# Kernel tuning notes

Measured on AMD Instinct MI355X. Metric: run time of the kernel, lower is better.

Reference implementation:

```python
import jax, jax.numpy as jnp
import numpy as np

HEADS = 8
EPS = 1e-4

def pixel_norm(x):
    # faithful to source: mean over dim=1 (token axis for [B,T,C] tensors)
    return x / jnp.sqrt(jnp.mean(x * x, axis=1, keepdims=True) + EPS)

def setup_inputs() -> dict:
    key = jax.random.key(0)
    ks = jax.random.split(key, 6)
    B, T, C = 4, 2048, 512
    s = 1.0 / np.sqrt(C)
    return {
        "hidden_states": jax.random.normal(ks[0], (B, T, C), jnp.float32),
        "Wq": jax.random.normal(ks[1], (C, C), jnp.float32) * s,
        "Wk": jax.random.normal(ks[2], (C, C), jnp.float32) * s,
        "Wv": jax.random.normal(ks[3], (C, C), jnp.float32) * s,
        "Wo": jax.random.normal(ks[4], (C, C), jnp.float32) * s,
        "bo": jnp.zeros((C,), jnp.float32),
    }

def reference(hidden_states, Wq, Wk, Wv, Wo, bo):
    B, T, C = hidden_states.shape
    H = HEADS
    d = C // H
    scale = 1.0 / np.sqrt(d)  # attn.scale = head_dim**-0.5
    residual = hidden_states

    q = pixel_norm(hidden_states @ Wq)  # [B,T,C]
    k = pixel_norm(hidden_states @ Wk)
    v = pixel_norm(hidden_states @ Wv)

    # head_to_batch_dim: [B,T,C] -> [B,H,T,d]
    def split_heads(x):
        return x.reshape(B, T, H, d).transpose(0, 2, 1, 3)
    q, k, v = split_heads(q), split_heads(k), split_heads(v)

    scores = jnp.einsum("bhqd,bhkd->bhqk", q, k) * scale
    probs = jax.nn.softmax(scores, axis=-1)
    out = jnp.einsum("bhqk,bhkd->bhqd", probs, v)  # [B,H,T,d]

    # batch_to_head_dim: [B,H,T,d] -> [B,T,C]
    out = out.transpose(0, 2, 1, 3).reshape(B, T, C)
    out = out @ Wo + bo  # to_out[0]; to_out[1] is dropout (identity in eval)
    out = out + residual  # residual_connection
    return out  # rescale_output_factor = 1.0
```

## Files before the change

### kernel.cpp

```cpp
#include <hip/hip_runtime.h>

#define Tt 2048
#define Cc 512
#define Bb 4
#define BC (Bb * Cc)

typedef __attribute__((ext_vector_type(4))) float f32x4;
typedef __attribute__((ext_vector_type(8))) _Float16 f16x8;
typedef __attribute__((ext_vector_type(4))) _Float16 f16x4;

__global__ __launch_bounds__(256) void wsetup(
    const float* __restrict__ Wq, const float* __restrict__ Wk,
    const float* __restrict__ Wv, const float* __restrict__ Wo,
    _Float16* __restrict__ Wt)
{
    const int z = blockIdx.y;
    const float* W = (z == 0) ? Wq : (z == 1) ? Wk : (z == 2) ? Wv : Wo;
    const int k0 = (blockIdx.x >> 3) * 64, n0 = (blockIdx.x & 7) * 64;
    const int tid = threadIdx.x;
    __shared__ float tile[64][65];

#pragma unroll
    for (int i = 0; i < 4; ++i) {
        const int idx = i * 256 + tid;
        const int kr = idx >> 4, c4 = idx & 15;
        float4 v = *(const float4*)&W[(size_t)(k0 + kr) * Cc + n0 + c4 * 4];
        tile[kr][c4 * 4 + 0] = v.x; tile[kr][c4 * 4 + 1] = v.y;
        tile[kr][c4 * 4 + 2] = v.z; tile[kr][c4 * 4 + 3] = v.w;
    }
    __syncthreads();
#pragma unroll
    for (int i = 0; i < 4; ++i) {
        const int idx = i * 256 + tid;
        const int nr = idx >> 4, k4 = idx & 15;
        f16x4 o;
        o[0] = (_Float16)tile[k4 * 4 + 0][nr];
        o[1] = (_Float16)tile[k4 * 4 + 1][nr];
        o[2] = (_Float16)tile[k4 * 4 + 2][nr];
        o[3] = (_Float16)tile[k4 * 4 + 3][nr];
        *(f16x4*)&Wt[((size_t)(z * 512 + n0 + nr)) * Cc + k0 + k4 * 4] = o;
    }
}

__global__ __launch_bounds__(256, 3) void qkv_mfma(
    const float* __restrict__ HS, const _Float16* __restrict__ Wt,
    _Float16* __restrict__ Qf, _Float16* __restrict__ Kf,
    _Float16* __restrict__ Vf, float* __restrict__ colsum)
{
    const int mt = blockIdx.x;
    const int nt = blockIdx.y;
    const int z  = blockIdx.z;
    _Float16* Out = (z == 0) ? Qf : (z == 1) ? Kf : Vf;

    const int tid = threadIdx.x;
    const int wave = tid >> 6, lane = tid & 63;
    const int quad = lane >> 4, lm = lane & 15;
    const int wm = (wave & 1) * 64, wn = (wave >> 1) * 64;

    __shared__ _Float16 sA[128 * 40];
    __shared__ _Float16 sB[128 * 40];

    f32x4 acc[4][4];
#pragma unroll
    for (int mf = 0; mf < 4; ++mf)
#pragma unroll
        for (int nf = 0; nf < 4; ++nf) acc[mf][nf] = (f32x4){0.f, 0.f, 0.f, 0.f};

    const int r2 = tid >> 1, kc = (tid & 1) * 16;
    const float* ga = HS + (size_t)(mt * 128 + r2) * Cc + kc;
    const _Float16* gb = Wt + ((size_t)(z * 512 + nt * 128 + r2)) * Cc + kc;

    for (int k0 = 0; k0 < Cc; k0 += 32) {
        __syncthreads();
        {
            float4 a0 = *(const float4*)&ga[k0];
            float4 a1 = *(const float4*)&ga[k0 + 4];
            float4 a2 = *(const float4*)&ga[k0 + 8];
            float4 a3 = *(const float4*)&ga[k0 + 12];
            f16x8 h0, h1;
            h0[0] = (_Float16)a0.x; h0[1] = (_Float16)a0.y;
            h0[2] = (_Float16)a0.z; h0[3] = (_Float16)a0.w;
            h0[4] = (_Float16)a1.x; h0[5] = (_Float16)a1.y;
            h0[6] = (_Float16)a1.z; h0[7] = (_Float16)a1.w;
            h1[0] = (_Float16)a2.x; h1[1] = (_Float16)a2.y;
            h1[2] = (_Float16)a2.z; h1[3] = (_Float16)a2.w;
            h1[4] = (_Float16)a3.x; h1[5] = (_Float16)a3.y;
            h1[6] = (_Float16)a3.z; h1[7] = (_Float16)a3.w;
            *(f16x8*)&sA[r2 * 40 + kc]     = h0;
            *(f16x8*)&sA[r2 * 40 + kc + 8] = h1;
            *(f16x8*)&sB[r2 * 40 + kc]     = *(const f16x8*)&gb[k0];
            *(f16x8*)&sB[r2 * 40 + kc + 8] = *(const f16x8*)&gb[k0 + 8];
        }
        __syncthreads();

        f16x8 ah[4], bh[4];
#pragma unroll
        for (int mf = 0; mf < 4; ++mf)
            ah[mf] = *(const f16x8*)&sA[(wm + mf * 16 + lm) * 40 + quad * 8];
#pragma unroll
        for (int nf = 0; nf < 4; ++nf)
            bh[nf] = *(const f16x8*)&sB[(wn + nf * 16 + lm) * 40 + quad * 8];
#pragma unroll
        for (int mf = 0; mf < 4; ++mf)
#pragma unroll
            for (int nf = 0; nf < 4; ++nf)
                acc[mf][nf] = __builtin_amdgcn_mfma_f32_16x16x32_f16(ah[mf], bh[nf], acc[mf][nf], 0, 0, 0);
    }

    const int bidx = mt >> 4;
#pragma unroll
    for (int nf = 0; nf < 4; ++nf) {
        float cs = 0.f;
#pragma unroll
        for (int mf = 0; mf < 4; ++mf)
#pragma unroll
            for (int r = 0; r < 4; ++r) {
                const float v = acc[mf][nf][r];
                const size_t idx =
                    (size_t)(mt * 128 + wm + mf * 16 + quad * 4 + r) * Cc +
                    nt * 128 + wn + nf * 16 + lm;
                Out[idx] = (_Float16)v;
                cs += v * v;
            }
        cs += __shfl_xor(cs, 16, 64);
        cs += __shfl_xor(cs, 32, 64);
        if (lane < 16)
            atomicAdd(&colsum[(size_t)z * BC + bidx * Cc + nt * 128 + wn + nf * 16 + lane], cs);
    }
}

__global__ void inv_norm_kernel(const float* __restrict__ colsum,
                                float* __restrict__ inv)
{
    const int i = blockIdx.x * blockDim.x + threadIdx.x;
    if (i < 3 * BC) inv[i] = rsqrtf(colsum[i] * (1.0f / Tt) + 1e-4f);
}

__global__ __launch_bounds__(256) void norm_vt(
    const _Float16* __restrict__ V, _Float16* __restrict__ VT)
{
    const int blk = blockIdx.x;
    const int b = blk >> 8, ct = (blk >> 5) & 7, tt = blk & 31;
    const int t0 = tt * 64, c0 = ct * 64;
    const int tid = threadIdx.x;

    __shared__ _Float16 tile[64 * 72];

#pragma unroll
    for (int i = 0; i < 2; ++i) {
        const int idx = i * 256 + tid;
        const int tr = idx >> 3, c8 = (idx & 7) * 8;
        *(f16x8*)&tile[tr * 72 + c8] =
            *(const f16x8*)&V[(size_t)(b * Tt + t0 + tr) * Cc + c0 + c8];
    }
    __syncthreads();
#pragma unroll
    for (int i = 0; i < 2; ++i) {
        const int idx = i * 256 + tid;
        const int cr = idx >> 3, t8 = (idx & 7) * 8;
        f16x8 o;
#pragma unroll
        for (int j = 0; j < 8; ++j) o[j] = tile[(t8 + j) * 72 + cr];
        *(f16x8*)&VT[(size_t)(b * Cc + c0 + cr) * Tt + t0 + t8] = o;
    }
}

#define LSTR 72

__global__ __launch_bounds__(256, 2) void attn_mfma(
    const _Float16* __restrict__ Qf, const _Float16* __restrict__ Kf,
    const _Float16* __restrict__ VT, const float* __restrict__ inv,
    _Float16* __restrict__ AO)
{
    const int qt = blockIdx.x;
    const int bh = blockIdx.y;
    const int b = bh >> 3, h = bh & 7;
    const int tid = threadIdx.x;
    const int wave = tid >> 6, lane = tid & 63;
    const int quad = lane >> 4, lm = lane & 15;

    __shared__ _Float16 sK[64 * LSTR];
    __shared__ _Float16 sVT[64 * LSTR];
    __shared__ _Float16 sP[4 * 32 * LSTR];
    _Float16* myP = sP + wave * 32 * LSTR;

    f16x8 qb[2][2];
    {
        const float* iqp = inv + b * Cc + h * 64;
        const float* ikp = inv + BC + b * Cc + h * 64;
#pragma unroll
        for (int qf = 0; qf < 2; ++qf) {
            const int row = qt * 128 + wave * 32 + qf * 16 + lm;
#pragma unroll
            for (int ks = 0; ks < 2; ++ks) {
                const int d0 = ks * 32 + quad * 8;
                f16x8 qv = *(const f16x8*)&Qf[(size_t)(b * Tt + row) * Cc + h * 64 + d0];
#pragma unroll
                for (int j = 0; j < 8; ++j) {
                    const float f = (float)qv[j] * iqp[d0 + j] * ikp[d0 + j] * 0.125f;
                    qb[qf][ks][j] = (_Float16)f;
                }
            }
        }
    }

    f32x4 o[4][2];
#pragma unroll
    for (int cf = 0; cf < 4; ++cf)
#pragma unroll
        for (int qf = 0; qf < 2; ++qf) o[cf][qf] = (f32x4){0.f, 0.f, 0.f, 0.f};
    float ls[2] = {0.f, 0.f};

    const int sr0 = tid >> 3, sc0 = (tid & 7) * 8;
    const int sr1 = sr0 + 32;
    const _Float16* gK = Kf + (size_t)b * Tt * Cc + h * 64;
    const _Float16* gV = VT + ((size_t)b * Cc + h * 64) * Tt;

    f16x8 rk0, rk1, rv0, rv1;
    {
        rk0 = *(const f16x8*)&gK[(size_t)sr0 * Cc + sc0];
        rk1 = *(const f16x8*)&gK[(size_t)sr1 * Cc + sc0];
        rv0 = *(const f16x8*)&gV[(size_t)sr0 * Tt + sc0];
        rv1 = *(const f16x8*)&gV[(size_t)sr1 * Tt + sc0];
    }

    for (int kt = 0; kt < 32; ++kt) {
        __syncthreads();
        *(f16x8*)&sK[sr0 * LSTR + sc0] = rk0;
        *(f16x8*)&sK[sr1 * LSTR + sc0] = rk1;
        *(f16x8*)&sVT[sr0 * LSTR + sc0] = rv0;
        *(f16x8*)&sVT[sr1 * LSTR + sc0] = rv1;
        __syncthreads();

        if (kt < 31) {
            const int t0 = (kt + 1) * 64;
            rk0 = *(const f16x8*)&gK[(size_t)(t0 + sr0) * Cc + sc0];
            rk1 = *(const f16x8*)&gK[(size_t)(t0 + sr1) * Cc + sc0];
            rv0 = *(const f16x8*)&gV[(size_t)sr0 * Tt + t0 + sc0];
            rv1 = *(const f16x8*)&gV[(size_t)sr1 * Tt + t0 + sc0];
        }

        f32x4 st[4][2];
#pragma unroll
        for (int kf = 0; kf < 4; ++kf)
#pragma unroll
            for (int qf = 0; qf < 2; ++qf) st[kf][qf] = (f32x4){0.f, 0.f, 0.f, 0.f};
#pragma unroll
        for (int ks = 0; ks < 2; ++ks) {
            f16x8 ka[4];
#pragma unroll
            for (int kf = 0; kf < 4; ++kf)
                ka[kf] = *(const f16x8*)&sK[(kf * 16 + lm) * LSTR + ks * 32 + quad * 8];
#pragma unroll
            for (int kf = 0; kf < 4; ++kf)
#pragma unroll
                for (int qf = 0; qf < 2; ++qf)
                    st[kf][qf] = __builtin_amdgcn_mfma_f32_16x16x32_f16(ka[kf], qb[qf][ks], st[kf][qf], 0, 0, 0);
        }

#pragma unroll
        for (int kf = 0; kf < 4; ++kf)
#pragma unroll
            for (int qf = 0; qf < 2; ++qf) {
                f16x4 pk;
#pragma unroll
                for (int r = 0; r < 4; ++r) {
                    const float p = __expf(st[kf][qf][r]);
                    ls[qf] += p;
                    pk[r] = (_Float16)p;
                }
                *(f16x4*)&myP[(qf * 16 + lm) * LSTR + kf * 16 + quad * 4] = pk;
            }

#pragma unroll
        for (int ks = 0; ks < 2; ++ks) {
            f16x8 pb[2];
#pragma unroll
            for (int qf = 0; qf < 2; ++qf)
                pb[qf] = *(const f16x8*)&myP[(qf * 16 + lm) * LSTR + ks * 32 + quad * 8];
            f16x8 va[4];
#pragma unroll
            for (int cf = 0; cf < 4; ++cf)
                va[cf] = *(const f16x8*)&sVT[(cf * 16 + lm) * LSTR + ks * 32 + quad * 8];
#pragma unroll
            for (int cf = 0; cf < 4; ++cf)
#pragma unroll
                for (int qf = 0; qf < 2; ++qf)
                    o[cf][qf] = __builtin_amdgcn_mfma_f32_16x16x32_f16(va[cf], pb[qf], o[cf][qf], 0, 0, 0);
        }
    }

    float il[2];
#pragma unroll
    for (int qf = 0; qf < 2; ++qf) {
        float s = ls[qf];
        s += __shfl_xor(s, 16, 64);
        s += __shfl_xor(s, 32, 64);
        il[qf] = 1.0f / s;
    }
    const float* ivp = inv + 2 * BC + b * Cc + h * 64;
    float iv[4][4];
#pragma unroll
    for (int cf = 0; cf < 4; ++cf) {
        float4 t = *(const float4*)&ivp[cf * 16 + quad * 4];
        iv[cf][0] = t.x; iv[cf][1] = t.y; iv[cf][2] = t.z; iv[cf][3] = t.w;
    }
#pragma unroll
    for (int qf = 0; qf < 2; ++qf) {
        const size_t row = (size_t)(b * Tt + qt * 128 + wave * 32 + qf * 16 + lm);
#pragma unroll
        for (int cf = 0; cf < 4; ++cf) {
            f16x4 pk;
#pragma unroll
            for (int r = 0; r < 4; ++r)
                pk[r] = (_Float16)(o[cf][qf][r] * il[qf] * iv[cf][r]);
            *(f16x4*)&AO[row * Cc + h * 64 + cf * 16 + quad * 4] = pk;
        }
    }
}

__global__ __launch_bounds__(256, 2) void out_mfma(
    const _Float16* __restrict__ AO, const _Float16* __restrict__ Wt,
    const float* __restrict__ bo, const float* __restrict__ HS,
    float* __restrict__ Outp)
{
    const int mt = blockIdx.x;
    const int nt = blockIdx.y;
    const int tid = threadIdx.x;
    const int wave = tid >> 6, lane = tid & 63;
    const int quad = lane >> 4, lm = lane & 15;
    const int wm = (wave & 1) * 32, wn = (wave >> 1) * 64;

    __shared__ _Float16 sA[64 * 40];
    __shared__ _Float16 sB[128 * 40];

    f32x4 acc[2][4];
#pragma unroll
    for (int mf = 0; mf < 2; ++mf)
#pragma unroll
        for (int nf = 0; nf < 4; ++nf) acc[mf][nf] = (f32x4){0.f, 0.f, 0.f, 0.f};

    const int ra = tid >> 2, ka = (tid & 3) * 8;
    const int rb = tid >> 1, kb = (tid & 1) * 16;
    const _Float16* gah = AO + (size_t)(mt * 64 + ra) * Cc + ka;
    const _Float16* gbh = Wt + ((size_t)(3 * 512 + nt * 128 + rb)) * Cc + kb;

    for (int k0 = 0; k0 < Cc; k0 += 32) {
        __syncthreads();
        {
            *(f16x8*)&sA[ra * 40 + ka] = *(const f16x8*)&gah[k0];
            *(f16x8*)&sB[rb * 40 + kb]     = *(const f16x8*)&gbh[k0];
            *(f16x8*)&sB[rb * 40 + kb + 8] = *(const f16x8*)&gbh[k0 + 8];
        }
        __syncthreads();

        f16x8 ah[2], bh[4];
#pragma unroll
        for (int mf = 0; mf < 2; ++mf)
            ah[mf] = *(const f16x8*)&sA[(wm + mf * 16 + lm) * 40 + quad * 8];
#pragma unroll
        for (int nf = 0; nf < 4; ++nf)
            bh[nf] = *(const f16x8*)&sB[(wn + nf * 16 + lm) * 40 + quad * 8];
#pragma unroll
        for (int mf = 0; mf < 2; ++mf)
#pragma unroll
            for (int nf = 0; nf < 4; ++nf)
                acc[mf][nf] = __builtin_amdgcn_mfma_f32_16x16x32_f16(ah[mf], bh[nf], acc[mf][nf], 0, 0, 0);
    }

#pragma unroll
    for (int mf = 0; mf < 2; ++mf)
#pragma unroll
        for (int r = 0; r < 4; ++r) {
            const size_t m = (size_t)(mt * 64 + wm + mf * 16 + quad * 4 + r);
#pragma unroll
            for (int nf = 0; nf < 4; ++nf) {
                const int col = nt * 128 + wn + nf * 16 + lm;
                Outp[m * Cc + col] = acc[mf][nf][r] + bo[col] + HS[m * Cc + col];
            }
        }
}

extern "C" void kernel_launch(void* const* d_in, const int* in_sizes, int n_in,
                              void* d_out, int out_size, void* d_ws,
                              size_t ws_size, hipStream_t stream)
{
    const float* HS = (const float*)d_in[0];
    const float* Wq = (const float*)d_in[1];
    const float* Wk = (const float*)d_in[2];
    const float* Wv = (const float*)d_in[3];
    const float* Wo = (const float*)d_in[4];
    const float* bo = (const float*)d_in[5];
    float* out = (float*)d_out;

    const size_t SZ = (size_t)Bb * Tt * Cc;
    _Float16* Qf  = (_Float16*)d_ws;
    _Float16* Kf  = Qf + SZ;
    _Float16* Vf  = Kf + SZ;
    _Float16* VTh = Vf + SZ;
    _Float16* AO  = VTh + SZ;
    _Float16* Wt  = AO + SZ;
    float* colsum = (float*)(Wt + 4 * Cc * Cc);
    float* inv    = colsum + 3 * BC;

    hipMemsetAsync(colsum, 0, 3 * BC * sizeof(float), stream);

    wsetup<<<dim3(64, 4), 256, 0, stream>>>(Wq, Wk, Wv, Wo, Wt);

    qkv_mfma<<<dim3(64, 4, 3), 256, 0, stream>>>(HS, Wt, Qf, Kf, Vf, colsum);

    inv_norm_kernel<<<(3 * BC + 255) / 256, 256, 0, stream>>>(colsum, inv);

    norm_vt<<<1024, 256, 0, stream>>>(Vf, VTh);

    attn_mfma<<<dim3(16, 32), 256, 0, stream>>>(Qf, Kf, VTh, inv, AO);

    out_mfma<<<dim3(128, 4), 256, 0, stream>>>(AO, Wt, bo, HS, out);
}
```

Baseline: 184.0 us.

## Use 8 waves of 16 query rows per attention block with exp2 softmax

The attention kernel now runs 512 threads per block, and each wave owns 16 query rows instead of 32. Per-thread accumulator and score registers are halved, and the block is declared for higher occupancy. The softmax switches to exp2, with log2(e) folded into the Q prescale, and uses packed round-toward-zero f16 conversion. In exchange, each K/V tile loaded into LDS is shared across more waves, but every wave reloads the V fragments for only half the MFMA work, and barriers now synchronize 8 waves.

```diff
diff --git a/kernel.cpp b/kernel.cpp
--- a/kernel.cpp
+++ b/kernel.cpp
@@ -8,6 +8,7 @@
 typedef __attribute__((ext_vector_type(4))) float f32x4;
 typedef __attribute__((ext_vector_type(8))) _Float16 f16x8;
 typedef __attribute__((ext_vector_type(4))) _Float16 f16x4;
+typedef __attribute__((ext_vector_type(2))) _Float16 f16x2;
 
 __global__ __launch_bounds__(256) void wsetup(
     const float* __restrict__ Wq, const float* __restrict__ Wk,
@@ -167,7 +168,7 @@
 
 #define LSTR 72
 
-__global__ __launch_bounds__(256, 2) void attn_mfma(
+__global__ __launch_bounds__(512, 4) void attn_mfma(
     const _Float16* __restrict__ Qf, const _Float16* __restrict__ Kf,
     const _Float16* __restrict__ VT, const float* __restrict__ inv,
     _Float16* __restrict__ AO)
@@ -181,70 +182,56 @@
 
     __shared__ _Float16 sK[64 * LSTR];
     __shared__ _Float16 sVT[64 * LSTR];
-    __shared__ _Float16 sP[4 * 32 * LSTR];
-    _Float16* myP = sP + wave * 32 * LSTR;
-
-    f16x8 qb[2][2];
+    __shared__ _Float16 sP[8 * 16 * LSTR];
+    _Float16* myP = sP + wave * 16 * LSTR;
+
+    f16x8 qb[2];
     {
         const float* iqp = inv + b * Cc + h * 64;
         const float* ikp = inv + BC + b * Cc + h * 64;
-#pragma unroll
-        for (int qf = 0; qf < 2; ++qf) {
-            const int row = qt * 128 + wave * 32 + qf * 16 + lm;
-#pragma unroll
-            for (int ks = 0; ks < 2; ++ks) {
-                const int d0 = ks * 32 + quad * 8;
-                f16x8 qv = *(const f16x8*)&Qf[(size_t)(b * Tt + row) * Cc + h * 64 + d0];
-#pragma unroll
-                for (int j = 0; j < 8; ++j) {
-                    const float f = (float)qv[j] * iqp[d0 + j] * ikp[d0 + j] * 0.125f;
-                    qb[qf][ks][j] = (_Float16)f;
-                }
+        const int row = qt * 128 + wave * 16 + lm;
+#pragma unroll
+        for (int ks = 0; ks < 2; ++ks) {
+            const int d0 = ks * 32 + quad * 8;
+            f16x8 qv = *(const f16x8*)&Qf[(size_t)(b * Tt + row) * Cc + h * 64 + d0];
+#pragma unroll
+            for (int j = 0; j < 8; ++j) {
+                const float f = (float)qv[j] * iqp[d0 + j] * ikp[d0 + j] * 0.18033688011f;
+                qb[ks][j] = (_Float16)f;
             }
         }
     }
 
-    f32x4 o[4][2];
-#pragma unroll
-    for (int cf = 0; cf < 4; ++cf)
-#pragma unroll
-        for (int qf = 0; qf < 2; ++qf) o[cf][qf] = (f32x4){0.f, 0.f, 0.f, 0.f};
-    float ls[2] = {0.f, 0.f};
-
-    const int sr0 = tid >> 3, sc0 = (tid & 7) * 8;
-    const int sr1 = sr0 + 32;
+    f32x4 o[4];
+#pragma unroll
+    for (int cf = 0; cf < 4; ++cf) o[cf] = (f32x4){0.f, 0.f, 0.f, 0.f};
+    float ls = 0.f;
+
+    const int sr = tid >> 3, sc = (tid & 7) * 8;
     const _Float16* gK = Kf + (size_t)b * Tt * Cc + h * 64;
     const _Float16* gV = VT + ((size_t)b * Cc + h * 64) * Tt;
 
-    f16x8 rk0, rk1, rv0, rv1;
+    f16x8 rk, rv;
     {
-        rk0 = *(const f16x8*)&gK[(size_t)sr0 * Cc + sc0];
-        rk1 = *(const f16x8*)&gK[(size_t)sr1 * Cc + sc0];
-        rv0 = *(const f16x8*)&gV[(size_t)sr0 * Tt + sc0];
-        rv1 = *(const f16x8*)&gV[(size_t)sr1 * Tt + sc0];
+        rk = *(const f16x8*)&gK[(size_t)sr * Cc + sc];
+        rv = *(const f16x8*)&gV[(size_t)sr * Tt + sc];
     }
 
     for (int kt = 0; kt < 32; ++kt) {
         __syncthreads();
-        *(f16x8*)&sK[sr0 * LSTR + sc0] = rk0;
-        *(f16x8*)&sK[sr1 * LSTR + sc0] = rk1;
-        *(f16x8*)&sVT[sr0 * LSTR + sc0] = rv0;
-        *(f16x8*)&sVT[sr1 * LSTR + sc0] = rv1;
+        *(f16x8*)&sK[sr * LSTR + sc] = rk;
+        *(f16x8*)&sVT[sr * LSTR + sc] = rv;
         __syncthreads();
 
         if (kt < 31) {
             const int t0 = (kt + 1) * 64;
-            rk0 = *(const f16x8*)&gK[(size_t)(t0 + sr0) * Cc + sc0];
-            rk1 = *(const f16x8*)&gK[(size_t)(t0 + sr1) * Cc + sc0];
-            rv0 = *(const f16x8*)&gV[(size_t)sr0 * Tt + t0 + sc0];
-            rv1 = *(const f16x8*)&gV[(size_t)sr1 * Tt + t0 + sc0];
-        }
-
-        f32x4 st[4][2];
-#pragma unroll
-        for (int kf = 0; kf < 4; ++kf)
-#pragma unroll
-            for (int qf = 0; qf < 2; ++qf) st[kf][qf] = (f32x4){0.f, 0.f, 0.f, 0.f};
+            rk = *(const f16x8*)&gK[(size_t)(t0 + sr) * Cc + sc];
+            rv = *(const f16x8*)&gV[(size_t)sr * Tt + t0 + sc];
+        }
+
+        f32x4 st[4];
+#pragma unroll
+        for (int kf = 0; kf < 4; ++kf) st[kf] = (f32x4){0.f, 0.f, 0.f, 0.f};
 #pragma unroll
         for (int ks = 0; ks < 2; ++ks) {
             f16x8 ka[4];
@@ -253,50 +240,42 @@
                 ka[kf] = *(const f16x8*)&sK[(kf * 16 + lm) * LSTR + ks * 32 + quad * 8];
 #pragma unroll
             for (int kf = 0; kf < 4; ++kf)
-#pragma unroll
-                for (int qf = 0; qf < 2; ++qf)
-                    st[kf][qf] = __builtin_amdgcn_mfma_f32_16x16x32_f16(ka[kf], qb[qf][ks], st[kf][qf], 0, 0, 0);
-        }
-
-#pragma unroll
-        for (int kf = 0; kf < 4; ++kf)
-#pragma unroll
-            for (int qf = 0; qf < 2; ++qf) {
-                f16x4 pk;
-#pragma unroll
-                for (int r = 0; r < 4; ++r) {
-                    const float p = __expf(st[kf][qf][r]);
-                    ls[qf] += p;
-                    pk[r] = (_Float16)p;
-                }
-                *(f16x4*)&myP[(qf * 16 + lm) * LSTR + kf * 16 + quad * 4] = pk;
-            }
+                st[kf] = __builtin_amdgcn_mfma_f32_16x16x32_f16(ka[kf], qb[ks], st[kf], 0, 0, 0);
+        }
+
+#pragma unroll
+        for (int kf = 0; kf < 4; ++kf) {
+            const float p0 = __builtin_amdgcn_exp2f(st[kf][0]);
+            const float p1 = __builtin_amdgcn_exp2f(st[kf][1]);
+            const float p2 = __builtin_amdgcn_exp2f(st[kf][2]);
+            const float p3 = __builtin_amdgcn_exp2f(st[kf][3]);
+            ls += (p0 + p1) + (p2 + p3);
+            const f16x2 lo = __builtin_bit_cast(f16x2, __builtin_amdgcn_cvt_pkrtz(p0, p1));
+            const f16x2 hi = __builtin_bit_cast(f16x2, __builtin_amdgcn_cvt_pkrtz(p2, p3));
+            f16x4 pk;
+            pk[0] = lo[0]; pk[1] = lo[1]; pk[2] = hi[0]; pk[3] = hi[1];
+            *(f16x4*)&myP[lm * LSTR + kf * 16 + quad * 4] = pk;
+        }
 
 #pragma unroll
         for (int ks = 0; ks < 2; ++ks) {
-            f16x8 pb[2];
-#pragma unroll
-            for (int qf = 0; qf < 2; ++qf)
-                pb[qf] = *(const f16x8*)&myP[(qf * 16 + lm) * LSTR + ks * 32 + quad * 8];
+            f16x8 pb = *(const f16x8*)&myP[lm * LSTR + ks * 32 + quad * 8];
             f16x8 va[4];
 #pragma unroll
             for (int cf = 0; cf < 4; ++cf)
                 va[cf] = *(const f16x8*)&sVT[(cf * 16 + lm) * LSTR + ks * 32 + quad * 8];
 #pragma unroll
             for (int cf = 0; cf < 4; ++cf)
-#pragma unroll
-                for (int qf = 0; qf < 2; ++qf)
-                    o[cf][qf] = __builtin_amdgcn_mfma_f32_16x16x32_f16(va[cf], pb[qf], o[cf][qf], 0, 0, 0);
-        }
-    }
-
-    float il[2];
-#pragma unroll
-    for (int qf = 0; qf < 2; ++qf) {
-        float s = ls[qf];
+                o[cf] = __builtin_amdgcn_mfma_f32_16x16x32_f16(va[cf], pb, o[cf], 0, 0, 0);
+        }
+    }
+
+    float il;
+    {
+        float s = ls;
         s += __shfl_xor(s, 16, 64);
         s += __shfl_xor(s, 32, 64);
-        il[qf] = 1.0f / s;
+        il = 1.0f / s;
     }
     const float* ivp = inv + 2 * BC + b * Cc + h * 64;
     float iv[4][4];
@@ -305,15 +284,14 @@
         float4 t = *(const float4*)&ivp[cf * 16 + quad * 4];
         iv[cf][0] = t.x; iv[cf][1] = t.y; iv[cf][2] = t.z; iv[cf][3] = t.w;
     }
-#pragma unroll
-    for (int qf = 0; qf < 2; ++qf) {
-        const size_t row = (size_t)(b * Tt + qt * 128 + wave * 32 + qf * 16 + lm);
+    {
+        const size_t row = (size_t)(b * Tt + qt * 128 + wave * 16 + lm);
 #pragma unroll
         for (int cf = 0; cf < 4; ++cf) {
             f16x4 pk;
 #pragma unroll
             for (int r = 0; r < 4; ++r)
-                pk[r] = (_Float16)(o[cf][qf][r] * il[qf] * iv[cf][r]);
+                pk[r] = (_Float16)(o[cf][r] * il * iv[cf][r]);
             *(f16x4*)&AO[row * Cc + h * 64 + cf * 16 + quad * 4] = pk;
         }
     }
@@ -403,7 +381,7 @@
     float* colsum = (float*)(Wt + 4 * Cc * Cc);
     float* inv    = colsum + 3 * BC;
 
-    hipMemsetAsync(colsum, 0, 3 * BC * sizeof(float), stream);
+    (void)hipMemsetAsync(colsum, 0, 3 * BC * sizeof(float), stream);
 
     wsetup<<<dim3(64, 4), 256, 0, stream>>>(Wq, Wk, Wv, Wo, Wt);
 
@@ -413,7 +391,7 @@
 
     norm_vt<<<1024, 256, 0, stream>>>(Vf, VTh);
 
-    attn_mfma<<<dim3(16, 32), 256, 0, stream>>>(Qf, Kf, VTh, inv, AO);
+    attn_mfma<<<dim3(16, 32), 512, 0, stream>>>(Qf, Kf, VTh, inv, AO);
 
     out_mfma<<<dim3(128, 4), 256, 0, stream>>>(AO, Wt, bo, HS, out);
 }
```

Result: slower. 189.1 us (+2.8%).

## Split attention key loop across two wave groups with LDS reduction, use exp2

Applied to the files above, without the earlier changes.

The attention block grows from 256 to 512 threads. Two groups of four waves each process alternating 64-key tiles for the same 128 queries, each with its own K/V shared buffers. The partial outputs and row sums are merged through shared memory at the end. Separately, the softmax scale is folded with log2(e) so exp2 can replace expf, and packed RTZ conversions build the fp16 probabilities. This doubles the waves working on the serial key loop, at the cost of more LDS, a final reduction step and possible occupancy limits.

```diff
diff --git a/kernel.cpp b/kernel.cpp
--- a/kernel.cpp
+++ b/kernel.cpp
@@ -8,6 +8,7 @@
 typedef __attribute__((ext_vector_type(4))) float f32x4;
 typedef __attribute__((ext_vector_type(8))) _Float16 f16x8;
 typedef __attribute__((ext_vector_type(4))) _Float16 f16x4;
+typedef __attribute__((ext_vector_type(2))) _Float16 f16x2;
 
 __global__ __launch_bounds__(256) void wsetup(
     const float* __restrict__ Wq, const float* __restrict__ Wk,
@@ -167,7 +168,7 @@
 
 #define LSTR 72
 
-__global__ __launch_bounds__(256, 2) void attn_mfma(
+__global__ __launch_bounds__(512, 4) void attn_mfma(
     const _Float16* __restrict__ Qf, const _Float16* __restrict__ Kf,
     const _Float16* __restrict__ VT, const float* __restrict__ inv,
     _Float16* __restrict__ AO)
@@ -177,12 +178,15 @@
     const int b = bh >> 3, h = bh & 7;
     const int tid = threadIdx.x;
     const int wave = tid >> 6, lane = tid & 63;
+    const int wg = wave & 3, grp = wave >> 2;
     const int quad = lane >> 4, lm = lane & 15;
 
-    __shared__ _Float16 sK[64 * LSTR];
-    __shared__ _Float16 sVT[64 * LSTR];
-    __shared__ _Float16 sP[4 * 32 * LSTR];
+    __shared__ _Float16 sK[2][64 * LSTR];
+    __shared__ _Float16 sVT[2][64 * LSTR];
+    __shared__ _Float16 sP[8 * 32 * LSTR];
     _Float16* myP = sP + wave * 32 * LSTR;
+    _Float16* sKg = sK[grp];
+    _Float16* sVg = sVT[grp];
 
     f16x8 qb[2][2];
     {
@@ -190,14 +194,14 @@
         const float* ikp = inv + BC + b * Cc + h * 64;
 #pragma unroll
         for (int qf = 0; qf < 2; ++qf) {
-            const int row = qt * 128 + wave * 32 + qf * 16 + lm;
+            const int row = qt * 128 + wg * 32 + qf * 16 + lm;
 #pragma unroll
             for (int ks = 0; ks < 2; ++ks) {
                 const int d0 = ks * 32 + quad * 8;
                 f16x8 qv = *(const f16x8*)&Qf[(size_t)(b * Tt + row) * Cc + h * 64 + d0];
 #pragma unroll
                 for (int j = 0; j < 8; ++j) {
-                    const float f = (float)qv[j] * iqp[d0 + j] * ikp[d0 + j] * 0.125f;
+                    const float f = (float)qv[j] * iqp[d0 + j] * ikp[d0 + j] * 0.18033688011f;
                     qb[qf][ks][j] = (_Float16)f;
                 }
             }
@@ -211,33 +215,35 @@
         for (int qf = 0; qf < 2; ++qf) o[cf][qf] = (f32x4){0.f, 0.f, 0.f, 0.f};
     float ls[2] = {0.f, 0.f};
 
-    const int sr0 = tid >> 3, sc0 = (tid & 7) * 8;
+    const int g256 = tid & 255;
+    const int sr0 = g256 >> 3, sc0 = (g256 & 7) * 8;
     const int sr1 = sr0 + 32;
     const _Float16* gK = Kf + (size_t)b * Tt * Cc + h * 64;
     const _Float16* gV = VT + ((size_t)b * Cc + h * 64) * Tt;
 
     f16x8 rk0, rk1, rv0, rv1;
     {
-        rk0 = *(const f16x8*)&gK[(size_t)sr0 * Cc + sc0];
-        rk1 = *(const f16x8*)&gK[(size_t)sr1 * Cc + sc0];
-        rv0 = *(const f16x8*)&gV[(size_t)sr0 * Tt + sc0];
-        rv1 = *(const f16x8*)&gV[(size_t)sr1 * Tt + sc0];
-    }
-
-    for (int kt = 0; kt < 32; ++kt) {
-        __syncthreads();
-        *(f16x8*)&sK[sr0 * LSTR + sc0] = rk0;
-        *(f16x8*)&sK[sr1 * LSTR + sc0] = rk1;
-        *(f16x8*)&sVT[sr0 * LSTR + sc0] = rv0;
-        *(f16x8*)&sVT[sr1 * LSTR + sc0] = rv1;
-        __syncthreads();
-
-        if (kt < 31) {
-            const int t0 = (kt + 1) * 64;
-            rk0 = *(const f16x8*)&gK[(size_t)(t0 + sr0) * Cc + sc0];
-            rk1 = *(const f16x8*)&gK[(size_t)(t0 + sr1) * Cc + sc0];
-            rv0 = *(const f16x8*)&gV[(size_t)sr0 * Tt + t0 + sc0];
-            rv1 = *(const f16x8*)&gV[(size_t)sr1 * Tt + t0 + sc0];
+        const int t0 = grp * 64;
+        rk0 = *(const f16x8*)&gK[(size_t)(t0 + sr0) * Cc + sc0];
+        rk1 = *(const f16x8*)&gK[(size_t)(t0 + sr1) * Cc + sc0];
+        rv0 = *(const f16x8*)&gV[(size_t)sr0 * Tt + t0 + sc0];
+        rv1 = *(const f16x8*)&gV[(size_t)sr1 * Tt + t0 + sc0];
+    }
+
+    for (int it = 0; it < 16; ++it) {
+        __syncthreads();
+        *(f16x8*)&sKg[sr0 * LSTR + sc0] = rk0;
+        *(f16x8*)&sKg[sr1 * LSTR + sc0] = rk1;
+        *(f16x8*)&sVg[sr0 * LSTR + sc0] = rv0;
+        *(f16x8*)&sVg[sr1 * LSTR + sc0] = rv1;
+        __syncthreads();
+
+        if (it < 15) {
+            const int tn = ((it + 1) * 2 + grp) * 64;
+            rk0 = *(const f16x8*)&gK[(size_t)(tn + sr0) * Cc + sc0];
+            rk1 = *(const f16x8*)&gK[(size_t)(tn + sr1) * Cc + sc0];
+            rv0 = *(const f16x8*)&gV[(size_t)sr0 * Tt + tn + sc0];
+            rv1 = *(const f16x8*)&gV[(size_t)sr1 * Tt + tn + sc0];
         }
 
         f32x4 st[4][2];
@@ -250,7 +256,7 @@
             f16x8 ka[4];
 #pragma unroll
             for (int kf = 0; kf < 4; ++kf)
-                ka[kf] = *(const f16x8*)&sK[(kf * 16 + lm) * LSTR + ks * 32 + quad * 8];
+                ka[kf] = *(const f16x8*)&sKg[(kf * 16 + lm) * LSTR + ks * 32 + quad * 8];
 #pragma unroll
             for (int kf = 0; kf < 4; ++kf)
 #pragma unroll
@@ -262,13 +268,15 @@
         for (int kf = 0; kf < 4; ++kf)
 #pragma unroll
             for (int qf = 0; qf < 2; ++qf) {
+                const float p0 = __builtin_amdgcn_exp2f(st[kf][qf][0]);
+                const float p1 = __builtin_amdgcn_exp2f(st[kf][qf][1]);
+                const float p2 = __builtin_amdgcn_exp2f(st[kf][qf][2]);
+                const float p3 = __builtin_amdgcn_exp2f(st[kf][qf][3]);
+                ls[qf] += (p0 + p1) + (p2 + p3);
+                const f16x2 lo = __builtin_bit_cast(f16x2, __builtin_amdgcn_cvt_pkrtz(p0, p1));
+                const f16x2 hi = __builtin_bit_cast(f16x2, __builtin_amdgcn_cvt_pkrtz(p2, p3));
                 f16x4 pk;
-#pragma unroll
-                for (int r = 0; r < 4; ++r) {
-                    const float p = __expf(st[kf][qf][r]);
-                    ls[qf] += p;
-                    pk[r] = (_Float16)p;
-                }
+                pk[0] = lo[0]; pk[1] = lo[1]; pk[2] = hi[0]; pk[3] = hi[1];
                 *(f16x4*)&myP[(qf * 16 + lm) * LSTR + kf * 16 + quad * 4] = pk;
             }
 
@@ -281,7 +289,7 @@
             f16x8 va[4];
 #pragma unroll
             for (int cf = 0; cf < 4; ++cf)
-                va[cf] = *(const f16x8*)&sVT[(cf * 16 + lm) * LSTR + ks * 32 + quad * 8];
+                va[cf] = *(const f16x8*)&sVg[(cf * 16 + lm) * LSTR + ks * 32 + quad * 8];
 #pragma unroll
             for (int cf = 0; cf < 4; ++cf)
 #pragma unroll
@@ -290,31 +298,56 @@
         }
     }
 
-    float il[2];
-#pragma unroll
-    for (int qf = 0; qf < 2; ++qf) {
-        float s = ls[qf];
-        s += __shfl_xor(s, 16, 64);
-        s += __shfl_xor(s, 32, 64);
-        il[qf] = 1.0f / s;
-    }
-    const float* ivp = inv + 2 * BC + b * Cc + h * 64;
-    float iv[4][4];
-#pragma unroll
-    for (int cf = 0; cf < 4; ++cf) {
-        float4 t = *(const float4*)&ivp[cf * 16 + quad * 4];
-        iv[cf][0] = t.x; iv[cf][1] = t.y; iv[cf][2] = t.z; iv[cf][3] = t.w;
-    }
-#pragma unroll
-    for (int qf = 0; qf < 2; ++qf) {
-        const size_t row = (size_t)(b * Tt + qt * 128 + wave * 32 + qf * 16 + lm);
+    float* fO = (float*)sP;
+    float* fL = (float*)sK;
+    __syncthreads();
+    if (grp == 1) {
+#pragma unroll
+        for (int cf = 0; cf < 4; ++cf)
+#pragma unroll
+            for (int qf = 0; qf < 2; ++qf)
+                *(f32x4*)&fO[wg * 2048 + (cf * 2 + qf) * 256 + lane * 4] = o[cf][qf];
+        fL[wg * 128 + lane] = ls[0];
+        fL[wg * 128 + 64 + lane] = ls[1];
+    }
+    __syncthreads();
+    if (grp == 0) {
+#pragma unroll
+        for (int cf = 0; cf < 4; ++cf)
+#pragma unroll
+            for (int qf = 0; qf < 2; ++qf) {
+                const f32x4 t = *(const f32x4*)&fO[wg * 2048 + (cf * 2 + qf) * 256 + lane * 4];
+                o[cf][qf] += t;
+            }
+        ls[0] += fL[wg * 128 + lane];
+        ls[1] += fL[wg * 128 + 64 + lane];
+
+        float il[2];
+#pragma unroll
+        for (int qf = 0; qf < 2; ++qf) {
+            float s = ls[qf];
+            s += __shfl_xor(s, 16, 64);
+            s += __shfl_xor(s, 32, 64);
+            il[qf] = 1.0f / s;
+        }
+        const float* ivp = inv + 2 * BC + b * Cc + h * 64;
+        float iv[4][4];
 #pragma unroll
         for (int cf = 0; cf < 4; ++cf) {
-            f16x4 pk;
-#pragma unroll
-            for (int r = 0; r < 4; ++r)
-                pk[r] = (_Float16)(o[cf][qf][r] * il[qf] * iv[cf][r]);
-            *(f16x4*)&AO[row * Cc + h * 64 + cf * 16 + quad * 4] = pk;
+            float4 t = *(const float4*)&ivp[cf * 16 + quad * 4];
+            iv[cf][0] = t.x; iv[cf][1] = t.y; iv[cf][2] = t.z; iv[cf][3] = t.w;
+        }
+#pragma unroll
+        for (int qf = 0; qf < 2; ++qf) {
+            const size_t row = (size_t)(b * Tt + qt * 128 + wg * 32 + qf * 16 + lm);
+#pragma unroll
+            for (int cf = 0; cf < 4; ++cf) {
+                f16x4 pk;
+#pragma unroll
+                for (int r = 0; r < 4; ++r)
+                    pk[r] = (_Float16)(o[cf][qf][r] * il[qf] * iv[cf][r]);
+                *(f16x4*)&AO[row * Cc + h * 64 + cf * 16 + quad * 4] = pk;
+            }
         }
     }
 }
@@ -403,7 +436,7 @@
     float* colsum = (float*)(Wt + 4 * Cc * Cc);
     float* inv    = colsum + 3 * BC;
 
-    hipMemsetAsync(colsum, 0, 3 * BC * sizeof(float), stream);
+    (void)hipMemsetAsync(colsum, 0, 3 * BC * sizeof(float), stream);
 
     wsetup<<<dim3(64, 4), 256, 0, stream>>>(Wq, Wk, Wv, Wo, Wt);
 
@@ -413,7 +446,7 @@
 
     norm_vt<<<1024, 256, 0, stream>>>(Vf, VTh);
 
-    attn_mfma<<<dim3(16, 32), 256, 0, stream>>>(Qf, Kf, VTh, inv, AO);
+    attn_mfma<<<dim3(16, 32), 512, 0, stream>>>(Qf, Kf, VTh, inv, AO);
 
     out_mfma<<<dim3(128, 4), 256, 0, stream>>>(AO, Wt, bo, HS, out);
 }
```

New measurement: 192.8 us. +4.8%, slower.

## Software-pipeline attention PV with double-buffered LDS, exp2 softmax, MFMA row sums

Applied to the files above, without the earlier changes.

Double-buffers the K, V^T and P tiles in shared memory so the P·V MFMAs for the previous key tile run after the QK^T MFMAs of the current tile. This lets the exponentials and matrix work of neighbouring tiles interleave. Folds log2(e) into the Q scale so it can use the hardware exp2, and packs probabilities to fp16 with cvt_pkrtz. Replaces the per-lane sum plus shuffle reduction with an MFMA against a ones vector. It also flattens the grid so consecutive blocks share the same query tile across heads. LDS use per block roughly doubles, which may limit occupancy, and round-to-zero fp16 conversion slightly changes numerics.

```diff
diff --git a/kernel.cpp b/kernel.cpp
--- a/kernel.cpp
+++ b/kernel.cpp
@@ -8,6 +8,7 @@
 typedef __attribute__((ext_vector_type(4))) float f32x4;
 typedef __attribute__((ext_vector_type(8))) _Float16 f16x8;
 typedef __attribute__((ext_vector_type(4))) _Float16 f16x4;
+typedef __attribute__((ext_vector_type(2))) _Float16 f16x2;
 
 __global__ __launch_bounds__(256) void wsetup(
     const float* __restrict__ Wq, const float* __restrict__ Wk,
@@ -172,17 +173,17 @@
     const _Float16* __restrict__ VT, const float* __restrict__ inv,
     _Float16* __restrict__ AO)
 {
-    const int qt = blockIdx.x;
-    const int bh = blockIdx.y;
+    const int bid = blockIdx.x;
+    const int qt = bid >> 5;
+    const int bh = bid & 31;
     const int b = bh >> 3, h = bh & 7;
     const int tid = threadIdx.x;
     const int wave = tid >> 6, lane = tid & 63;
     const int quad = lane >> 4, lm = lane & 15;
 
-    __shared__ _Float16 sK[64 * LSTR];
-    __shared__ _Float16 sVT[64 * LSTR];
-    __shared__ _Float16 sP[4 * 32 * LSTR];
-    _Float16* myP = sP + wave * 32 * LSTR;
+    __shared__ _Float16 sK[2][64 * LSTR];
+    __shared__ _Float16 sVT[2][64 * LSTR];
+    __shared__ _Float16 sP[2][4][32 * LSTR];
 
     f16x8 qb[2][2];
     {
@@ -197,7 +198,7 @@
                 f16x8 qv = *(const f16x8*)&Qf[(size_t)(b * Tt + row) * Cc + h * 64 + d0];
 #pragma unroll
                 for (int j = 0; j < 8; ++j) {
-                    const float f = (float)qv[j] * iqp[d0 + j] * ikp[d0 + j] * 0.125f;
+                    const float f = (float)qv[j] * iqp[d0 + j] * ikp[d0 + j] * 0.18033688011f;
                     qb[qf][ks][j] = (_Float16)f;
                 }
             }
@@ -209,7 +210,12 @@
     for (int cf = 0; cf < 4; ++cf)
 #pragma unroll
         for (int qf = 0; qf < 2; ++qf) o[cf][qf] = (f32x4){0.f, 0.f, 0.f, 0.f};
-    float ls[2] = {0.f, 0.f};
+    f32x4 ol[2];
+#pragma unroll
+    for (int qf = 0; qf < 2; ++qf) ol[qf] = (f32x4){0.f, 0.f, 0.f, 0.f};
+    f16x8 ones;
+#pragma unroll
+    for (int j = 0; j < 8; ++j) ones[j] = (_Float16)1.0f;
 
     const int sr0 = tid >> 3, sc0 = (tid & 7) * 8;
     const int sr1 = sr0 + 32;
@@ -225,11 +231,17 @@
     }
 
     for (int kt = 0; kt < 32; ++kt) {
-        __syncthreads();
-        *(f16x8*)&sK[sr0 * LSTR + sc0] = rk0;
-        *(f16x8*)&sK[sr1 * LSTR + sc0] = rk1;
-        *(f16x8*)&sVT[sr0 * LSTR + sc0] = rv0;
-        *(f16x8*)&sVT[sr1 * LSTR + sc0] = rv1;
+        const int cur = kt & 1, prv = cur ^ 1;
+        _Float16* sKc = sK[cur];
+        _Float16* sVc = sVT[cur];
+        _Float16* myPc = &sP[cur][wave][0];
+        _Float16* myPp = &sP[prv][wave][0];
+
+        __syncthreads();
+        *(f16x8*)&sKc[sr0 * LSTR + sc0] = rk0;
+        *(f16x8*)&sKc[sr1 * LSTR + sc0] = rk1;
+        *(f16x8*)&sVc[sr0 * LSTR + sc0] = rv0;
+        *(f16x8*)&sVc[sr1 * LSTR + sc0] = rv1;
         __syncthreads();
 
         if (kt < 31) {
@@ -250,7 +262,7 @@
             f16x8 ka[4];
 #pragma unroll
             for (int kf = 0; kf < 4; ++kf)
-                ka[kf] = *(const f16x8*)&sK[(kf * 16 + lm) * LSTR + ks * 32 + quad * 8];
+                ka[kf] = *(const f16x8*)&sKc[(kf * 16 + lm) * LSTR + ks * 32 + quad * 8];
 #pragma unroll
             for (int kf = 0; kf < 4; ++kf)
 #pragma unroll
@@ -258,46 +270,72 @@
                     st[kf][qf] = __builtin_amdgcn_mfma_f32_16x16x32_f16(ka[kf], qb[qf][ks], st[kf][qf], 0, 0, 0);
         }
 
+        if (kt > 0) {
+            _Float16* sVp = sVT[prv];
+#pragma unroll
+            for (int ks = 0; ks < 2; ++ks) {
+                f16x8 pb[2];
+#pragma unroll
+                for (int qf = 0; qf < 2; ++qf)
+                    pb[qf] = *(const f16x8*)&myPp[(qf * 16 + lm) * LSTR + ks * 32 + quad * 8];
+                f16x8 va[4];
+#pragma unroll
+                for (int cf = 0; cf < 4; ++cf)
+                    va[cf] = *(const f16x8*)&sVp[(cf * 16 + lm) * LSTR + ks * 32 + quad * 8];
+#pragma unroll
+                for (int cf = 0; cf < 4; ++cf)
+#pragma unroll
+                    for (int qf = 0; qf < 2; ++qf)
+                        o[cf][qf] = __builtin_amdgcn_mfma_f32_16x16x32_f16(va[cf], pb[qf], o[cf][qf], 0, 0, 0);
+#pragma unroll
+                for (int qf = 0; qf < 2; ++qf)
+                    ol[qf] = __builtin_amdgcn_mfma_f32_16x16x32_f16(ones, pb[qf], ol[qf], 0, 0, 0);
+            }
+        }
+
 #pragma unroll
         for (int kf = 0; kf < 4; ++kf)
 #pragma unroll
             for (int qf = 0; qf < 2; ++qf) {
+                const float p0 = __builtin_amdgcn_exp2f(st[kf][qf][0]);
+                const float p1 = __builtin_amdgcn_exp2f(st[kf][qf][1]);
+                const float p2 = __builtin_amdgcn_exp2f(st[kf][qf][2]);
+                const float p3 = __builtin_amdgcn_exp2f(st[kf][qf][3]);
+                const f16x2 lo = __builtin_bit_cast(f16x2, __builtin_amdgcn_cvt_pkrtz(p0, p1));
+                const f16x2 hi = __builtin_bit_cast(f16x2, __builtin_amdgcn_cvt_pkrtz(p2, p3));
                 f16x4 pk;
-#pragma unroll
-                for (int r = 0; r < 4; ++r) {
-                    const float p = __expf(st[kf][qf][r]);
-                    ls[qf] += p;
-                    pk[r] = (_Float16)p;
-                }
-                *(f16x4*)&myP[(qf * 16 + lm) * LSTR + kf * 16 + quad * 4] = pk;
+                pk[0] = lo[0]; pk[1] = lo[1]; pk[2] = hi[0]; pk[3] = hi[1];
+                *(f16x4*)&myPc[(qf * 16 + lm) * LSTR + kf * 16 + quad * 4] = pk;
             }
-
+    }
+
+    {
+        _Float16* myPp = &sP[1][wave][0];
+        _Float16* sVp = sVT[1];
 #pragma unroll
         for (int ks = 0; ks < 2; ++ks) {
             f16x8 pb[2];
 #pragma unroll
             for (int qf = 0; qf < 2; ++qf)
-                pb[qf] = *(const f16x8*)&myP[(qf * 16 + lm) * LSTR + ks * 32 + quad * 8];
+                pb[qf] = *(const f16x8*)&myPp[(qf * 16 + lm) * LSTR + ks * 32 + quad * 8];
             f16x8 va[4];
 #pragma unroll
             for (int cf = 0; cf < 4; ++cf)
-                va[cf] = *(const f16x8*)&sVT[(cf * 16 + lm) * LSTR + ks * 32 + quad * 8];
+                va[cf] = *(const f16x8*)&sVp[(cf * 16 + lm) * LSTR + ks * 32 + quad * 8];
 #pragma unroll
             for (int cf = 0; cf < 4; ++cf)
 #pragma unroll
                 for (int qf = 0; qf < 2; ++qf)
                     o[cf][qf] = __builtin_amdgcn_mfma_f32_16x16x32_f16(va[cf], pb[qf], o[cf][qf], 0, 0, 0);
+#pragma unroll
+            for (int qf = 0; qf < 2; ++qf)
+                ol[qf] = __builtin_amdgcn_mfma_f32_16x16x32_f16(ones, pb[qf], ol[qf], 0, 0, 0);
         }
     }
 
     float il[2];
 #pragma unroll
-    for (int qf = 0; qf < 2; ++qf) {
-        float s = ls[qf];
-        s += __shfl_xor(s, 16, 64);
-        s += __shfl_xor(s, 32, 64);
-        il[qf] = 1.0f / s;
-    }
+    for (int qf = 0; qf < 2; ++qf) il[qf] = 1.0f / ol[qf][0];
     const float* ivp = inv + 2 * BC + b * Cc + h * 64;
     float iv[4][4];
 #pragma unroll
@@ -403,7 +441,7 @@
     float* colsum = (float*)(Wt + 4 * Cc * Cc);
     float* inv    = colsum + 3 * BC;
 
-    hipMemsetAsync(colsum, 0, 3 * BC * sizeof(float), stream);
+    (void)hipMemsetAsync(colsum, 0, 3 * BC * sizeof(float), stream);
 
     wsetup<<<dim3(64, 4), 256, 0, stream>>>(Wq, Wk, Wv, Wo, Wt);
 
@@ -413,7 +451,7 @@
 
     norm_vt<<<1024, 256, 0, stream>>>(Vf, VTh);
 
-    attn_mfma<<<dim3(16, 32), 256, 0, stream>>>(Qf, Kf, VTh, inv, AO);
+    attn_mfma<<<dim3(512), 256, 0, stream>>>(Qf, Kf, VTh, inv, AO);
 
     out_mfma<<<dim3(128, 4), 256, 0, stream>>>(AO, Wt, bo, HS, out);
 }
```

After: 181.6 us. Within noise of the previous version (-1.3%).
